# Performance work log

Hardware: AMD Instinct MI355X
Metric: run time of the kernel (lower is better)

## Reference

```python
import jax, jax.numpy as jnp
import numpy as np


def conv2d(x, w, b, pad):
    out = jax.lax.conv_general_dilated(x, w, (1, 1), ((pad, pad), (pad, pad)),
                                       dimension_numbers=('NCHW', 'OIHW', 'NCHW'))
    return out + b[None, :, None, None]


def silu(x):
    return x * jax.nn.sigmoid(x)


def group_norm(x, g, b, groups, eps=1e-5):
    B, C, H, W = x.shape
    xg = x.reshape(B, groups, C // groups, H, W)
    m = xg.mean(axis=(2, 3, 4), keepdims=True)
    v = xg.var(axis=(2, 3, 4), keepdims=True)
    xg = (xg - m) * jax.lax.rsqrt(v + eps)
    return xg.reshape(B, C, H, W) * g[None, :, None, None] + b[None, :, None, None]


def snake_cumsum(off):
    # off: [B,K,H,W]. Center kernel point has zero offset; points accumulate
    # outward from center (the 'snake' bend), as in DSCNet.
    K = off.shape[1]
    c = K // 2
    upper = jnp.cumsum(off[:, c + 1:], axis=1)
    lower = jnp.flip(jnp.cumsum(jnp.flip(off[:, :c], axis=1), axis=1), axis=1)
    return jnp.concatenate([lower, jnp.zeros_like(off[:, :1]), upper], axis=1)


def bilinear_gather(img, ys, xs):
    # img [B,C,H,W]; ys,xs [B,K,H,W] float coords -> sampled [B,C,K,H,W]
    B, C, H, W = img.shape
    K = ys.shape[1]
    ys = jnp.clip(ys, 0.0, H - 1.0)
    xs = jnp.clip(xs, 0.0, W - 1.0)
    y0f = jnp.floor(ys)
    x0f = jnp.floor(xs)
    wy = (ys - y0f)[:, None]  # [B,1,K,H,W]
    wx = (xs - x0f)[:, None]
    y0 = y0f.astype(jnp.int32)
    x0 = x0f.astype(jnp.int32)
    y1 = jnp.minimum(y0 + 1, H - 1)
    x1 = jnp.minimum(x0 + 1, W - 1)
    flat = img.reshape(B, C, H * W)

    def gat(yi, xi):
        idx = (yi * W + xi).reshape(B, -1)  # [B, K*H*W]
        g = jnp.take_along_axis(flat, idx[:, None, :], axis=2)
        return g.reshape(B, C, K, H, W)

    return (gat(y0, x0) * (1 - wy) * (1 - wx) + gat(y0, x1) * (1 - wy) * wx
            + gat(y1, x0) * wy * (1 - wx) + gat(y1, x1) * wy * wx)


def dsconv(x, off_w, off_b, dsc_w, dsc_b, gn_g, gn_b, morph, extend_scope=1.0):
    # Dynamic snake conv for one morphology.
    # morph 0: kernel spreads along x, bends in y; morph 1: opposite.
    B, C, H, W = x.shape
    K = dsc_w.shape[-1]
    c = K // 2
    off = jnp.tanh(conv2d(x, off_w, off_b, pad=1))  # [B,2K,H,W]; BN folded into conv bias
    bend = snake_cumsum(off[:, :K] if morph == 0 else off[:, K:])  # [B,K,H,W]
    spread = (jnp.arange(K) - c).astype(x.dtype)[None, :, None, None]
    hh = jnp.arange(H, dtype=x.dtype)[None, None, :, None]
    ww = jnp.arange(W, dtype=x.dtype)[None, None, None, :]
    if morph == 0:
        ys = hh + extend_scope * bend
        xs = jnp.broadcast_to(ww + spread, ys.shape)
    else:
        xs = ww + extend_scope * bend
        ys = jnp.broadcast_to(hh + spread, xs.shape)
    sampled = bilinear_gather(x, ys, xs)  # [B,C,K,H,W]
    # k-point conv over the stacked snake axis == (K,1)/(1,K) conv with stride K
    out = jnp.einsum('bckhw,ock->bohw', sampled, dsc_w) + dsc_b[None, :, None, None]
    O = dsc_w.shape[0]
    return jax.nn.relu(group_norm(out, gn_g, gn_b, groups=O // 4))


def dysnake_conv(x, p):
    # DySnakeConv: standard conv + snake-x + snake-y, concat, 1x1 fuse
    kpad = p['conv0_w'].shape[-1] // 2
    a = silu(conv2d(x, p['conv0_w'], p['conv0_b'], pad=kpad))
    bx = dsconv(x, p['offx_w'], p['offx_b'], p['dscx_w'], p['dscx_b'], p['gnx_g'], p['gnx_b'], morph=0)
    by = dsconv(x, p['offy_w'], p['offy_b'], p['dscy_w'], p['dscy_b'], p['gny_g'], p['gny_b'], morph=1)
    cat = jnp.concatenate([a, bx, by], axis=1)  # [B,3*ouc,H,W]
    return silu(jnp.einsum('bchw,oc->bohw', cat, p['fuse_w']) + p['fuse_b'][None, :, None, None])


_PNAMES = ['conv0_w', 'conv0_b', 'offx_w', 'offx_b', 'dscx_w', 'dscx_b', 'gnx_g', 'gnx_b',
           'offy_w', 'offy_b', 'dscy_w', 'dscy_b', 'gny_g', 'gny_b', 'fuse_w', 'fuse_b']


def setup_inputs() -> dict:
    key = jax.random.key(0)
    ks = iter(jax.random.split(key, 64))

    def rn(shape, s=0.05):
        return jax.random.normal(next(ks), shape, dtype=jnp.float32) * s

    B, H, W = 8, 80, 80
    c1, c2, c_ = 256, 256, 128
    kk = 3

    def block(inc, ouc, pre):
        return {
            pre + 'conv0_w': rn((ouc, inc, kk, kk)), pre + 'conv0_b': rn((ouc,)),
            pre + 'offx_w': rn((2 * kk, inc, 3, 3)), pre + 'offx_b': rn((2 * kk,)),
            pre + 'dscx_w': rn((ouc, inc, kk)), pre + 'dscx_b': rn((ouc,)),
            pre + 'gnx_g': jnp.ones((ouc,), jnp.float32), pre + 'gnx_b': jnp.zeros((ouc,), jnp.float32),
            pre + 'offy_w': rn((2 * kk, inc, 3, 3)), pre + 'offy_b': rn((2 * kk,)),
            pre + 'dscy_w': rn((ouc, inc, kk)), pre + 'dscy_b': rn((ouc,)),
            pre + 'gny_g': jnp.ones((ouc,), jnp.float32), pre + 'gny_b': jnp.zeros((ouc,), jnp.float32),
            pre + 'fuse_w': rn((ouc, 3 * ouc)), pre + 'fuse_b': rn((ouc,)),
        }

    inp = {'x': jax.random.normal(next(ks), (B, c1, H, W), dtype=jnp.float32)}
    inp.update(block(c1, c_, 'cv1_'))
    inp.update(block(c_, c2, 'cv2_'))
    return inp


def reference(x, cv1_conv0_w, cv1_conv0_b, cv1_offx_w, cv1_offx_b, cv1_dscx_w, cv1_dscx_b,
              cv1_gnx_g, cv1_gnx_b, cv1_offy_w, cv1_offy_b, cv1_dscy_w, cv1_dscy_b,
              cv1_gny_g, cv1_gny_b, cv1_fuse_w, cv1_fuse_b,
              cv2_conv0_w, cv2_conv0_b, cv2_offx_w, cv2_offx_b, cv2_dscx_w, cv2_dscx_b,
              cv2_gnx_g, cv2_gnx_b, cv2_offy_w, cv2_offy_b, cv2_dscy_w, cv2_dscy_b,
              cv2_gny_g, cv2_gny_b, cv2_fuse_w, cv2_fuse_b):
    p1 = dict(zip(_PNAMES, (cv1_conv0_w, cv1_conv0_b, cv1_offx_w, cv1_offx_b, cv1_dscx_w, cv1_dscx_b,
                            cv1_gnx_g, cv1_gnx_b, cv1_offy_w, cv1_offy_b, cv1_dscy_w, cv1_dscy_b,
                            cv1_gny_g, cv1_gny_b, cv1_fuse_w, cv1_fuse_b)))
    p2 = dict(zip(_PNAMES, (cv2_conv0_w, cv2_conv0_b, cv2_offx_w, cv2_offx_b, cv2_dscx_w, cv2_dscx_b,
                            cv2_gnx_g, cv2_gnx_b, cv2_offy_w, cv2_offy_b, cv2_dscy_w, cv2_dscy_b,
                            cv2_gny_g, cv2_gny_b, cv2_fuse_w, cv2_fuse_b)))
    h = dysnake_conv(x, p1)
    h = dysnake_conv(h, p2)
    return x + h  # shortcut and c1 == c2
```

## Files before the change

kernel.cpp:

```cpp
#include <hip/hip_runtime.h>
#include <cstddef>

#define B_   8
#define H_   80
#define W_   80
#define HW   6400
#define W2   82
#define HW2  6724

typedef __attribute__((ext_vector_type(8)))  short short8;
typedef __attribute__((ext_vector_type(16))) float f32x16;

__device__ __forceinline__ float bf2f(ushort u) {
    return __uint_as_float(((unsigned)u) << 16);
}
__device__ __forceinline__ ushort f2bf(float f) {
    unsigned u = __float_as_uint(f);
    u += 0x7FFF + ((u >> 16) & 1);
    return (ushort)(u >> 16);
}
__device__ __forceinline__ f32x16 mfma16(short8 a, short8 b, f32x16 c) {
    return __builtin_amdgcn_mfma_f32_32x32x16_bf16(a, b, c, 0, 0, 0);
}
__device__ __forceinline__ void async16(const void* g, void* l) {
    __builtin_amdgcn_global_load_lds(
        (const __attribute__((address_space(1))) unsigned int*)g,
        (__attribute__((address_space(3))) unsigned int*)l, 16, 0, 0);
}
__device__ __forceinline__ const ushort* frag_ptr(const ushort* sbuf, int row, int c8l) {
    return sbuf + row * 64 + ((c8l ^ (row & 7)) << 3);
}

__global__ __launch_bounds__(256) void halo_zero2_kernel(
    ushort* __restrict__ xp1, ushort* __restrict__ xp2) {
    int idx = blockIdx.x * 256 + threadIdx.x;
    const int n1 = B_ * 324 * 32;
    const int n2 = B_ * 324 * 16;
    ushort* xp; int C, slots, i;
    if (idx < n1) { xp = xp1; C = 256; slots = 32; i = idx; }
    else if (idx < n1 + n2) { xp = xp2; C = 128; slots = 16; i = idx - n1; }
    else return;
    int sl = i % slots;
    int t = i / slots;
    int p = t % 324;
    int b = t / 324;
    int h, w;
    if (p < 164) { h = (p < 82) ? 0 : 81; w = p % 82; }
    else { int q = p - 164; w = (q < 80) ? 0 : 81; h = 1 + (q % 80); }
    *(uint4*)(xp + ((size_t)(b * HW2 + h * W2 + w)) * C + sl * 8) =
        make_uint4(0, 0, 0, 0);
}

__global__ __launch_bounds__(256) void transpose_x_kernel(
    const float* __restrict__ x, ushort* __restrict__ xp, int C) {
    __shared__ float s[64][65];
    int hw0 = blockIdx.x * 64, c0 = blockIdx.y * 64, b = blockIdx.z;
    int t = threadIdx.x;
    int hl = t & 63, cq = t >> 6;
    #pragma unroll
    for (int i = 0; i < 16; i++) {
        int cl = cq * 16 + i;
        s[cl][hl] = x[((size_t)(b * C + c0 + cl)) * HW + hw0 + hl];
    }
    __syncthreads();
    int cl = t & 63, hq = t >> 6;
    #pragma unroll
    for (int i = 0; i < 16; i++) {
        int hl2 = hq * 16 + i;
        int hw = hw0 + hl2;
        int h = hw / W_, w = hw - h * W_;
        xp[((size_t)(b * HW2 + (h + 1) * W2 + w + 1)) * C + c0 + cl] = f2bf(s[cl][hl2]);
    }
}

__global__ __launch_bounds__(256) void final_add_kernel(
    const float* __restrict__ x, const ushort* __restrict__ h2,
    float* __restrict__ out, int C) {
    __shared__ float s[64][65];
    int hw0 = blockIdx.x * 64, c0 = blockIdx.y * 64, b = blockIdx.z;
    int t = threadIdx.x;
    int cl = t & 63, hq = t >> 6;
    #pragma unroll
    for (int i = 0; i < 16; i++) {
        int hl = hq * 16 + i;
        s[cl][hl] = bf2f(h2[((size_t)(b * HW + hw0 + hl)) * C + c0 + cl]);
    }
    __syncthreads();
    int hl = t & 63, cq = t >> 6;
    #pragma unroll
    for (int i = 0; i < 16; i++) {
        int cl2 = cq * 16 + i;
        size_t o = ((size_t)(b * C + c0 + cl2)) * HW + hw0 + hl;
        out[o] = x[o] + s[cl2][hl];
    }
}

struct WJobs {
    const float* src[8];
    ushort* dst[8];
    int cin[8], t[8];
    int start[9];
};

__global__ __launch_bounds__(256) void wprep_all_kernel(WJobs J) {
    int idx = blockIdx.x * 256 + threadIdx.x;
    if (idx >= J.start[8]) return;
    int j = 0;
    #pragma unroll
    for (int k = 1; k < 8; k++) if (idx >= J.start[k]) j = k;
    int i = idx - J.start[j];
    int CIN = J.cin[j], T = J.t[j];
    int oc = i / (CIN * T);
    int r = i - oc * CIN * T;
    int ci = r / T, t_ = r - ci * T;
    J.dst[j][((size_t)oc * T + t_) * CIN + ci] = f2bf(J.src[j][i]);
}

__global__ void wprep_off_kernel(const float* __restrict__ wx_,
                                 const float* __restrict__ bx_,
                                 const float* __restrict__ wy_,
                                 const float* __restrict__ by_,
                                 ushort* __restrict__ dst,
                                 float* __restrict__ bdst, int CIN) {
    int idx = blockIdx.x * 256 + threadIdx.x;
    if (idx < 4) {
        const int chs[4] = {0, 2, 3, 5};
        bdst[idx] = (idx < 2) ? bx_[chs[idx]] : by_[chs[idx]];
    }
    if (idx >= 32 * 9 * CIN) return;
    int oc = idx / (9 * CIN);
    int r = idx - oc * 9 * CIN;
    int tap = r / CIN, ci = r - tap * CIN;
    float v = 0.f;
    if (oc < 4) {
        const int chs[4] = {0, 2, 3, 5};
        const float* src = (oc < 2) ? wx_ : wy_;
        v = src[((size_t)chs[oc] * CIN + ci) * 9 + tap];
    }
    dst[idx] = f2bf(v);
}

__global__ __launch_bounds__(256, 2) void off_conv_mfma_kernel(
    const ushort* __restrict__ xp, const ushort* __restrict__ wB,
    const float* __restrict__ bias, float* __restrict__ off4, int CIN) {
    __shared__ ushort s_x[162 * 64];
    __shared__ ushort s_w[144 * 64];
    int tid = threadIdx.x;
    int ty0 = (blockIdx.x / 5) * 16, tx0 = (blockIdx.x % 5) * 16;
    int b = blockIdx.y;
    int lane = tid & 63, wid = tid >> 6;
    int l31 = lane & 31, kg = lane >> 5;
    int pym[2], pxm[2];
    #pragma unroll
    for (int mf = 0; mf < 2; mf++) {
        int p = wid * 64 + mf * 32 + l31;
        pym[mf] = p >> 4; pxm[mf] = p & 15;
    }
    f32x16 acc[2] = {};
    for (int c0 = 0; c0 < CIN; c0 += 32) {
        __syncthreads();
        for (int u = tid; u < 1296; u += 256) {
            int pid = u >> 2, ci8 = u & 3;
            int r = pid / 18, c = pid - r * 18;
            int py = ty0 + r, px = tx0 + c;
            uint4 v = *(const uint4*)(xp + ((size_t)(b * HW2 + py * W2 + px)) * CIN
                                      + c0 + ci8 * 8);
            int row = pid >> 1;
            int phys = (((pid & 1) << 2) + ci8) ^ (row & 7);
            *(uint4*)(s_x + row * 64 + phys * 8) = v;
        }
        for (int cc = wid; cc < 18; cc += 4) {
            int L = cc * 64 + lane;
            int row = L >> 3, phys = L & 7;
            int logical = phys ^ (row & 7);
            int tap = row >> 4, ocp = row & 15;
            int oc = ocp * 2 + (logical >> 2), ci8 = logical & 3;
            async16(wB + ((size_t)oc * 9 + tap) * CIN + c0 + ci8 * 8,
                    s_w + (size_t)L * 8);
        }
        __syncthreads();
        #pragma unroll
        for (int tap = 0; tap < 9; tap++) {
            int dy = tap / 3, dx = tap - dy * 3;
            int wrow = tap * 16 + (l31 >> 1);
            #pragma unroll
            for (int ks = 0; ks < 2; ks++) {
                int blk = ks * 2 + kg;
                int wphys = (((l31 & 1) << 2) + blk) ^ (wrow & 7);
                short8 bfr = *(const short8*)(s_w + wrow * 64 + wphys * 8);
                #pragma unroll
                for (int mf = 0; mf < 2; mf++) {
                    int pix = (pym[mf] + dy) * 18 + (pxm[mf] + dx);
                    int xrow = pix >> 1;
                    int xphys = (((pix & 1) << 2) + blk) ^ (xrow & 7);
                    short8 afr = *(const short8*)(s_x + xrow * 64 + xphys * 8);
                    acc[mf] = mfma16(afr, bfr, acc[mf]);
                }
            }
        }
    }
    int oc = l31;
    if (oc < 4) {
        float bb = bias[oc];
        #pragma unroll
        for (int mf = 0; mf < 2; mf++) {
            #pragma unroll
            for (int reg = 0; reg < 16; reg++) {
                int row = (reg & 3) + 8 * (reg >> 2) + 4 * kg;
                int p = wid * 64 + mf * 32 + row;
                int y = ty0 + (p >> 4), x = tx0 + (p & 15);
                off4[((size_t)b * 4 + oc) * HW + y * W_ + x] = tanhf(acc[mf][reg] + bb);
            }
        }
    }
}

__global__ __launch_bounds__(256, 4) void convdsc_kernel(
    const ushort* __restrict__ xp,
    const ushort* __restrict__ wC, const float* __restrict__ biasC,
    ushort* __restrict__ outC,
    const float* __restrict__ off4,
    const ushort* __restrict__ Bwx, const float* __restrict__ biasx,
    ushort* __restrict__ outx,
    const ushort* __restrict__ Bwy, const float* __restrict__ biasy,
    ushort* __restrict__ outy, float* __restrict__ stat, int CIN, int OC) {
    __shared__ ushort s_a[128 * 64];
    __shared__ ushort s_b[128 * 64];
    __shared__ int   s_i0[3][128];
    __shared__ int   s_i1[3][128];
    __shared__ float s_wl[3][128];
    int tid = threadIdx.x;
    int m0 = blockIdx.x * 128, n0 = blockIdx.y * 128;
    int b = m0 / HW, hw0 = m0 - b * HW;
    int lane = tid & 63, wid = tid >> 6;
    int l31 = lane & 31, kg = lane >> 5;
    int wm = wid >> 1, wn = wid & 1;

    if (blockIdx.z == 0) {
        const ushort* xpb = xp + (size_t)b * HW2 * CIN;
        const ushort* asrc[4];
        #pragma unroll
        for (int j = 0; j < 4; j++) {
            int s = (wid * 4 + j) * 64 + lane;
            int r = s >> 3, c8p = s & 7;
            int c8l = c8p ^ (r & 7);
            int hw = hw0 + r;
            int h = hw / W_, w = hw - h * W_;
            asrc[j] = xpb + ((size_t)((h + 1) * W2 + (w + 1))) * CIN + c8l * 8;
        }
        f32x16 acc[2][2] = {};
        int K = 9 * CIN, nk = K >> 6;
        int tap = 0, cioff = 0;
        for (int kc = 0; kc < nk; kc++) {
            int kg64 = kc << 6;
            int dy = tap / 3, dx = tap - dy * 3;
            int soff = ((dy - 1) * W2 + (dx - 1)) * CIN + cioff;
            __syncthreads();
            #pragma unroll
            for (int j = 0; j < 4; j++) {
                int s = (wid * 4 + j) * 64 + lane;
                int r = s >> 3, c8p = s & 7;
                int c8l = c8p ^ (r & 7);
                async16(wC + (size_t)(n0 + r) * K + kg64 + c8l * 8, s_b + s * 8);
                async16(asrc[j] + soff, s_a + s * 8);
            }
            __syncthreads();
            #pragma unroll
            for (int ks = 0; ks < 4; ks++) {
                int c8l = ks * 2 + kg;
                short8 af0 = *(const short8*)frag_ptr(s_a, wm * 64 + l31, c8l);
                short8 af1 = *(const short8*)frag_ptr(s_a, wm * 64 + 32 + l31, c8l);
                short8 bf0 = *(const short8*)frag_ptr(s_b, wn * 64 + l31, c8l);
                short8 bf1 = *(const short8*)frag_ptr(s_b, wn * 64 + 32 + l31, c8l);
                acc[0][0] = mfma16(af0, bf0, acc[0][0]);
                acc[0][1] = mfma16(af0, bf1, acc[0][1]);
                acc[1][0] = mfma16(af1, bf0, acc[1][0]);
                acc[1][1] = mfma16(af1, bf1, acc[1][1]);
            }
            cioff += 64;
            if (cioff == CIN) { cioff = 0; tap++; }
        }
        #pragma unroll
        for (int nf = 0; nf < 2; nf++) {
            int n = n0 + wn * 64 + nf * 32 + l31;
            float bb = biasC[n];
            #pragma unroll
            for (int mf = 0; mf < 2; mf++) {
                #pragma unroll
                for (int reg = 0; reg < 16; reg++) {
                    int row = (reg & 3) + 8 * (reg >> 2) + 4 * kg;
                    int m = m0 + wm * 64 + mf * 32 + row;
                    float v = acc[mf][nf][reg] + bb;
                    v = v / (1.f + expf(-v));
                    outC[(size_t)m * OC + n] = f2bf(v);
                }
            }
        }
        return;
    }

    int morph = blockIdx.z - 1;
    const ushort* Bw = morph ? Bwy : Bwx;
    const float* bias = morph ? biasy : biasx;
    ushort* out = morph ? outy : outx;
    float* statm = stat + (size_t)morph * B_ * 256 * 2;
    for (int u = tid; u < 384; u += 256) {
        int k3 = u >> 7, r = u & 127;
        int hw = hw0 + r;
        int h = hw / W_, w = hw - h * W_;
        float bend = 0.f;
        if (k3 != 1) {
            int mp = (morph ? 2 : 0) + (k3 >> 1);
            bend = off4[((size_t)b * 4 + mp) * HW + hw];
        }
        int i0, i1; float wl;
        if (morph == 0) {
            float ys = fminf(fmaxf((float)h + bend, 0.f), 79.f);
            float y0f = floorf(ys); wl = ys - y0f;
            int y0 = (int)y0f, y1 = min(y0 + 1, 79);
            int xk = min(max(w + k3 - 1, 0), 79);
            i0 = (y0 + 1) * W2 + xk + 1; i1 = (y1 + 1) * W2 + xk + 1;
        } else {
            float xs = fminf(fmaxf((float)w + bend, 0.f), 79.f);
            float x0f = floorf(xs); wl = xs - x0f;
            int x0 = (int)x0f, x1 = min(x0 + 1, 79);
            int yk = min(max(h + k3 - 1, 0), 79);
            i0 = (yk + 1) * W2 + x0 + 1; i1 = (yk + 1) * W2 + x1 + 1;
        }
        s_i0[k3][r] = i0; s_i1[k3][r] = i1; s_wl[k3][r] = wl;
    }
    const ushort* xb = xp + (size_t)b * HW2 * CIN;
    const ushort* asrcC[4];
    #pragma unroll
    for (int j = 0; j < 4; j++) {
        int s = (wid * 4 + j) * 64 + lane;
        int r = s >> 3, c8p = s & 7;
        int c8l = c8p ^ (r & 7);
        int hw = hw0 + r;
        int h = hw / W_, w = hw - h * W_;
        asrcC[j] = xb + ((size_t)((h + 1) * W2 + (w + 1))) * CIN + c8l * 8;
    }
    f32x16 acc[2][2] = {};
    int K = 3 * CIN, nk = K >> 6;
    for (int kc = 0; kc < nk; kc++) {
        int kg64 = kc << 6;
        int k3 = kg64 / CIN;
        int cioff = kg64 - k3 * CIN;
        __syncthreads();
        #pragma unroll
        for (int j = 0; j < 4; j++) {
            int s = (wid * 4 + j) * 64 + lane;
            int r = s >> 3, c8p = s & 7;
            int c8l = c8p ^ (r & 7);
            async16(Bw + (size_t)(n0 + r) * K + kg64 + c8l * 8, s_b + s * 8);
        }
        if (k3 == 1) {
            #pragma unroll
            for (int j = 0; j < 4; j++) {
                int s = (wid * 4 + j) * 64 + lane;
                async16(asrcC[j] + cioff, s_a + s * 8);
            }
        } else {
            #pragma unroll
            for (int i = 0; i < 4; i++) {
                int s = i * 256 + tid;
                int r = s >> 3, c8p = s & 7;
                int c8l = c8p ^ (r & 7);
                int ci = cioff + c8l * 8;
                float wl = s_wl[k3][r];
                uint4 u0 = *(const uint4*)(xb + (size_t)s_i0[k3][r] * CIN + ci);
                uint4 u1 = *(const uint4*)(xb + (size_t)s_i1[k3][r] * CIN + ci);
                const ushort* p0 = (const ushort*)&u0;
                const ushort* p1 = (const ushort*)&u1;
                uint ov[4];
                #pragma unroll
                for (int j = 0; j < 4; j++) {
                    float a0 = bf2f(p0[2 * j]),     b0 = bf2f(p1[2 * j]);
                    float a1 = bf2f(p0[2 * j + 1]), b1 = bf2f(p1[2 * j + 1]);
                    float r0 = a0 + (b0 - a0) * wl;
                    float r1 = a1 + (b1 - a1) * wl;
                    asm("v_cvt_pk_bf16_f32 %0, %1, %2"
                        : "=v"(ov[j]) : "v"(r0), "v"(r1));
                }
                *(uint4*)(s_a + s * 8) = *(uint4*)ov;
            }
        }
        __syncthreads();
        #pragma unroll
        for (int ks = 0; ks < 4; ks++) {
            int c8l = ks * 2 + kg;
            short8 af0 = *(const short8*)frag_ptr(s_a, wm * 64 + l31, c8l);
            short8 af1 = *(const short8*)frag_ptr(s_a, wm * 64 + 32 + l31, c8l);
            short8 bf0 = *(const short8*)frag_ptr(s_b, wn * 64 + l31, c8l);
            short8 bf1 = *(const short8*)frag_ptr(s_b, wn * 64 + 32 + l31, c8l);
            acc[0][0] = mfma16(af0, bf0, acc[0][0]);
            acc[0][1] = mfma16(af0, bf1, acc[0][1]);
            acc[1][0] = mfma16(af1, bf0, acc[1][0]);
            acc[1][1] = mfma16(af1, bf1, acc[1][1]);
        }
    }
    #pragma unroll
    for (int nf = 0; nf < 2; nf++) {
        int n = n0 + wn * 64 + nf * 32 + l31;
        float bb = bias[n];
        float ssum = 0.f, ssq = 0.f;
        #pragma unroll
        for (int mf = 0; mf < 2; mf++) {
            #pragma unroll
            for (int reg = 0; reg < 16; reg++) {
                int row = (reg & 3) + 8 * (reg >> 2) + 4 * kg;
                int m = m0 + wm * 64 + mf * 32 + row;
                float v = acc[mf][nf][reg] + bb;
                ssum += v; ssq += v * v;
                out[(size_t)m * OC + n] = f2bf(v);
            }
        }
        ssum += __shfl_xor(ssum, 32);
        ssq  += __shfl_xor(ssq, 32);
        if (kg == 0) {
            float* st = statm + ((size_t)b * OC + n) * 2;
            atomicAdd(st, ssum);
            atomicAdd(st + 1, ssq);
        }
    }
}

__global__ __launch_bounds__(256, 4) void gemm128_kernel(
    const ushort* __restrict__ a0, const ushort* __restrict__ a1,
    const ushort* __restrict__ a2, int part_k,
    const ushort* __restrict__ Bw, int K, int N,
    const float* __restrict__ bias, ushort* __restrict__ out, int epi_silu,
    int out_pad) {
    __shared__ ushort s_a[128 * 64];
    __shared__ ushort s_b[128 * 64];
    int tid = threadIdx.x;
    int m0 = blockIdx.x * 128, n0 = blockIdx.y * 128;
    int lane = tid & 63, wid = tid >> 6;
    int l31 = lane & 31, kg = lane >> 5;
    int wm = wid >> 1, wn = wid & 1;
    f32x16 acc[2][2] = {};
    int nk = K >> 6;
    for (int kc = 0; kc < nk; kc++) {
        int kg64 = kc << 6;
        int part = kg64 / part_k;
        int koff = kg64 - part * part_k;
        const ushort* ap = (part == 0) ? a0 : (part == 1 ? a1 : a2);
        __syncthreads();
        #pragma unroll
        for (int j = 0; j < 4; j++) {
            int s = (wid * 4 + j) * 64 + lane;
            int r = s >> 3, c8p = s & 7;
            int c8l = c8p ^ (r & 7);
            async16(ap + (size_t)(m0 + r) * part_k + koff + c8l * 8, s_a + s * 8);
            async16(Bw + (size_t)(n0 + r) * K + kg64 + c8l * 8, s_b + s * 8);
        }
        __syncthreads();
        #pragma unroll
        for (int ks = 0; ks < 4; ks++) {
            int c8l = ks * 2 + kg;
            short8 af0 = *(const short8*)frag_ptr(s_a, wm * 64 + l31, c8l);
            short8 af1 = *(const short8*)frag_ptr(s_a, wm * 64 + 32 + l31, c8l);
            short8 bf0 = *(const short8*)frag_ptr(s_b, wn * 64 + l31, c8l);
            short8 bf1 = *(const short8*)frag_ptr(s_b, wn * 64 + 32 + l31, c8l);
            acc[0][0] = mfma16(af0, bf0, acc[0][0]);
            acc[0][1] = mfma16(af0, bf1, acc[0][1]);
            acc[1][0] = mfma16(af1, bf0, acc[1][0]);
            acc[1][1] = mfma16(af1, bf1, acc[1][1]);
        }
    }
    #pragma unroll
    for (int nf = 0; nf < 2; nf++) {
        int n = n0 + wn * 64 + nf * 32 + l31;
        float bb = bias[n];
        #pragma unroll
        for (int mf = 0; mf < 2; mf++) {
            #pragma unroll
            for (int reg = 0; reg < 16; reg++) {
                int row = (reg & 3) + 8 * (reg >> 2) + 4 * kg;
                int m = m0 + wm * 64 + mf * 32 + row;
                float v = acc[mf][nf][reg] + bb;
                if (epi_silu) v = v / (1.f + expf(-v));
                size_t mm = (size_t)m;
                if (out_pad) {
                    int bb_ = m / HW, hw = m - bb_ * HW;
                    int h = hw / W_, w = hw - h * W_;
                    mm = (size_t)bb_ * HW2 + (h + 1) * W2 + w + 1;
                }
                out[mm * N + n] = f2bf(v);
            }
        }
    }
}

__global__ void gn_finalize_kernel(const float* __restrict__ stat,
                                   const float* __restrict__ gx,
                                   const float* __restrict__ bx,
                                   const float* __restrict__ gy,
                                   const float* __restrict__ by,
                                   float* __restrict__ scx, float* __restrict__ shx,
                                   float* __restrict__ scy, float* __restrict__ shy,
                                   int C) {
    int idx = blockIdx.x * 256 + threadIdx.x;
    if (idx >= B_ * C) return;
    int which = blockIdx.y;
    const float* gamma = which ? gy : gx;
    const float* beta  = which ? by : bx;
    float* sc = which ? scy : scx;
    float* sh = which ? shy : shx;
    int b = idx / C, c = idx - b * C;
    const float* st = stat + (size_t)which * B_ * 256 * 2
                    + ((size_t)b * C + (c & ~3)) * 2;
    float s  = st[0] + st[2] + st[4] + st[6];
    float sq = st[1] + st[3] + st[5] + st[7];
    float mean = s / (4.f * HW);
    float var = sq / (4.f * HW) - mean * mean;
    float rs = rsqrtf(var + 1e-5f);
    float scale = rs * gamma[c];
    sc[idx] = scale;
    sh[idx] = beta[c] - mean * scale;
}

__global__ __launch_bounds__(256) void gn_apply_kernel(
    ushort* __restrict__ bqx, ushort* __restrict__ bqy,
    const float* __restrict__ scx, const float* __restrict__ shx,
    const float* __restrict__ scy, const float* __restrict__ shy, int C) {
    ushort* bq = blockIdx.y ? bqy : bqx;
    const float* sc = blockIdx.y ? scy : scx;
    const float* sh = blockIdx.y ? shy : shx;
    size_t e = ((size_t)blockIdx.x * 256 + threadIdx.x) * 8;
    int c = (int)(e % C);
    int b = (int)(e / ((size_t)HW * C));
    const float* scb = sc + (size_t)b * C + c;
    const float* shb = sh + (size_t)b * C + c;
    uint4 v = *(const uint4*)(bq + e);
    const ushort* sv = (const ushort*)&v;
    ushort tv[8];
    #pragma unroll
    for (int j = 0; j < 8; j++)
        tv[j] = f2bf(fmaxf(bf2f(sv[j]) * scb[j] + shb[j], 0.f));
    *(uint4*)(bq + e) = *(uint4*)tv;
}

struct BlkBuf {
    ushort *xp, *abuf, *bqx, *bqy, *hout;
    float *off4, *stat, *scx, *shx, *scy, *shy, *boff;
    ushort *wc, *wdx, *wdy, *wf, *woff;
};

static void run_block(const BlkBuf& B, int CIN, int OC,
                      const float* const* P, int out_pad, hipStream_t stream) {
    dim3 blk(256);
    hipMemsetAsync(B.stat, 0, (size_t)2 * B_ * 256 * 2 * 4, stream);
    off_conv_mfma_kernel<<<dim3(25, B_), blk, 0, stream>>>(
        B.xp, B.woff, B.boff, B.off4, CIN);
    convdsc_kernel<<<dim3(400, OC / 128, 3), blk, 0, stream>>>(
        B.xp, B.wc, P[1], B.abuf,
        B.off4, B.wdx, P[5], B.bqx, B.wdy, P[11], B.bqy, B.stat, CIN, OC);
    int fgrid = (B_ * OC + 255) / 256;
    gn_finalize_kernel<<<dim3(fgrid, 2), blk, 0, stream>>>(
        B.stat, P[6], P[7], P[12], P[13], B.scx, B.shx, B.scy, B.shy, OC);
    gn_apply_kernel<<<dim3((B_ * HW * OC) / 2048, 2), blk, 0, stream>>>(
        B.bqx, B.bqy, B.scx, B.shx, B.scy, B.shy, OC);
    gemm128_kernel<<<dim3(400, OC / 128), blk, 0, stream>>>(
        B.abuf, B.bqx, B.bqy, OC, B.wf, 3 * OC, OC, P[15], B.hout, 1, out_pad);
}

extern "C" void kernel_launch(void* const* d_in, const int* in_sizes, int n_in,
                              void* d_out, int out_size, void* d_ws, size_t ws_size,
                              hipStream_t stream) {
    const float* x = (const float*)d_in[0];
    const float* P1[16];
    const float* P2[16];
    for (int i = 0; i < 16; i++) {
        P1[i] = (const float*)d_in[1 + i];
        P2[i] = (const float*)d_in[17 + i];
    }
    char* base = (char*)d_ws;
    size_t off = 0;
    auto alloc = [&](size_t bytes) -> char* {
        off = (off + 255) & ~(size_t)255;
        char* p = base + off;
        off += bytes;
        return p;
    };
    ushort* xp1  = (ushort*)alloc((size_t)B_ * HW2 * 256 * 2);
    ushort* xp2  = (ushort*)alloc((size_t)B_ * HW2 * 128 * 2);
    ushort* abuf = (ushort*)alloc((size_t)B_ * HW * 256 * 2);
    ushort* bqx  = (ushort*)alloc((size_t)B_ * HW * 256 * 2);
    ushort* bqy  = (ushort*)alloc((size_t)B_ * HW * 256 * 2);
    float*  off4 = (float*)alloc((size_t)B_ * 4 * HW * 4);
    float*  stat = (float*)alloc((size_t)2 * B_ * 256 * 2 * 4);
    float*  scx  = (float*)alloc(B_ * 256 * 4);
    float*  shx  = (float*)alloc(B_ * 256 * 4);
    float*  scy  = (float*)alloc(B_ * 256 * 4);
    float*  shy  = (float*)alloc(B_ * 256 * 4);
    ushort* wc1  = (ushort*)alloc((size_t)128 * 9 * 256 * 2);
    ushort* wc2  = (ushort*)alloc((size_t)256 * 9 * 128 * 2);
    ushort* wdx1 = (ushort*)alloc((size_t)128 * 3 * 256 * 2);
    ushort* wdy1 = (ushort*)alloc((size_t)128 * 3 * 256 * 2);
    ushort* wdx2 = (ushort*)alloc((size_t)256 * 3 * 128 * 2);
    ushort* wdy2 = (ushort*)alloc((size_t)256 * 3 * 128 * 2);
    ushort* wf1  = (ushort*)alloc((size_t)128 * 384 * 2);
    ushort* wf2  = (ushort*)alloc((size_t)256 * 768 * 2);
    ushort* wo1  = (ushort*)alloc((size_t)32 * 9 * 256 * 2);
    ushort* wo2  = (ushort*)alloc((size_t)32 * 9 * 128 * 2);
    float*  bo1  = (float*)alloc(32 * 4);
    float*  bo2  = (float*)alloc(32 * 4);
    ushort* h2 = xp1;

    dim3 blk(256);
    {
        int total = B_ * 324 * 32 + B_ * 324 * 16;
        halo_zero2_kernel<<<(total + 255) / 256, blk, 0, stream>>>(xp1, xp2);
    }

    {
        WJobs J;
        const float* srcs[8] = {P1[0], P1[4], P1[10], P1[14],
                                P2[0], P2[4], P2[10], P2[14]};
        ushort* dsts[8] = {wc1, wdx1, wdy1, wf1, wc2, wdx2, wdy2, wf2};
        int cins[8] = {256, 256, 256, 384, 128, 128, 128, 768};
        int ts[8]   = {9, 3, 3, 1, 9, 3, 3, 1};
        int ocs[8]  = {128, 128, 128, 128, 256, 256, 256, 256};
        int acc = 0;
        for (int j = 0; j < 8; j++) {
            J.src[j] = srcs[j]; J.dst[j] = dsts[j];
            J.cin[j] = cins[j]; J.t[j] = ts[j];
            J.start[j] = acc;
            acc += ocs[j] * cins[j] * ts[j];
        }
        J.start[8] = acc;
        wprep_all_kernel<<<(acc + 255) / 256, blk, 0, stream>>>(J);
    }
    wprep_off_kernel<<<(32 * 9 * 256 + 255) / 256, blk, 0, stream>>>(
        P1[2], P1[3], P1[8], P1[9], wo1, bo1, 256);
    wprep_off_kernel<<<(32 * 9 * 128 + 255) / 256, blk, 0, stream>>>(
        P2[2], P2[3], P2[8], P2[9], wo2, bo2, 128);

    transpose_x_kernel<<<dim3(100, 4, B_), blk, 0, stream>>>(x, xp1, 256);

    BlkBuf B1 = {xp1, abuf, bqx, bqy, xp2, off4, stat, scx, shx, scy, shy,
                 bo1, wc1, wdx1, wdy1, wf1, wo1};
    run_block(B1, 256, 128, P1, 1, stream);

    BlkBuf B2 = {xp2, abuf, bqx, bqy, h2, off4, stat, scx, shx, scy, shy,
                 bo2, wc2, wdx2, wdy2, wf2, wo2};
    run_block(B2, 128, 256, P2, 0, stream);

    final_add_kernel<<<dim3(100, 4, B_), blk, 0, stream>>>(x, h2, (float*)d_out, 256);
}
```

Measured before the change: 522.1 us.

## Fuse group-norm apply into fuse GEMM A-load and keep snake indices in registers

Removes the separate gn_apply pass by applying the GroupNorm scale/shift and ReLU while the fuse GEMM loads the bqx/bqy parts into LDS, replacing async copies with synchronous load-transform-store for those K chunks. In convdsc, the per-row bilinear indices and weights move from shared arrays into registers computed per thread, and the occupancy hint rises from 4 to 5 blocks. This saves a full read-modify-write of the two branch activations, at the cost of losing async overlap for two thirds of the GEMM K loop and added register pressure.

After: 669.8 us. 28.3% more time.

```diff
diff --git a/kernel.cpp b/kernel.cpp
--- a/kernel.cpp
+++ b/kernel.cpp
@@ -215,7 +215,7 @@
     }
 }
 
-__global__ __launch_bounds__(256, 4) void convdsc_kernel(
+__global__ __launch_bounds__(256, 5) void convdsc_kernel(
     const ushort* __restrict__ xp,
     const ushort* __restrict__ wC, const float* __restrict__ biasC,
     ushort* __restrict__ outC,
@@ -226,9 +226,6 @@
     ushort* __restrict__ outy, float* __restrict__ stat, int CIN, int OC) {
     __shared__ ushort s_a[128 * 64];
     __shared__ ushort s_b[128 * 64];
-    __shared__ int   s_i0[3][128];
-    __shared__ int   s_i1[3][128];
-    __shared__ float s_wl[3][128];
     int tid = threadIdx.x;
     int m0 = blockIdx.x * 128, n0 = blockIdx.y * 128;
     int b = m0 / HW, hw0 = m0 - b * HW;
@@ -304,30 +301,35 @@
     const float* bias = morph ? biasy : biasx;
     ushort* out = morph ? outy : outx;
     float* statm = stat + (size_t)morph * B_ * 256 * 2;
-    for (int u = tid; u < 384; u += 256) {
-        int k3 = u >> 7, r = u & 127;
+    int i0a[4], i1a[4], i0c[4], i1c[4];
+    float wla[4], wlc[4];
+    #pragma unroll
+    for (int i = 0; i < 4; i++) {
+        int r = i * 32 + (tid >> 3);
         int hw = hw0 + r;
         int h = hw / W_, w = hw - h * W_;
-        float bend = 0.f;
-        if (k3 != 1) {
-            int mp = (morph ? 2 : 0) + (k3 >> 1);
-            bend = off4[((size_t)b * 4 + mp) * HW + hw];
-        }
-        int i0, i1; float wl;
-        if (morph == 0) {
-            float ys = fminf(fmaxf((float)h + bend, 0.f), 79.f);
-            float y0f = floorf(ys); wl = ys - y0f;
-            int y0 = (int)y0f, y1 = min(y0 + 1, 79);
-            int xk = min(max(w + k3 - 1, 0), 79);
-            i0 = (y0 + 1) * W2 + xk + 1; i1 = (y1 + 1) * W2 + xk + 1;
-        } else {
-            float xs = fminf(fmaxf((float)w + bend, 0.f), 79.f);
-            float x0f = floorf(xs); wl = xs - x0f;
-            int x0 = (int)x0f, x1 = min(x0 + 1, 79);
-            int yk = min(max(h + k3 - 1, 0), 79);
-            i0 = (yk + 1) * W2 + x0 + 1; i1 = (yk + 1) * W2 + x1 + 1;
-        }
-        s_i0[k3][r] = i0; s_i1[k3][r] = i1; s_wl[k3][r] = wl;
+        #pragma unroll
+        for (int kk = 0; kk < 2; kk++) {
+            int k3v = kk * 2;
+            int mp = (morph ? 2 : 0) + (k3v >> 1);
+            float bend = off4[((size_t)b * 4 + mp) * HW + hw];
+            int i0, i1; float wl;
+            if (morph == 0) {
+                float ys = fminf(fmaxf((float)h + bend, 0.f), 79.f);
+                float y0f = floorf(ys); wl = ys - y0f;
+                int y0 = (int)y0f, y1 = min(y0 + 1, 79);
+                int xk = min(max(w + k3v - 1, 0), 79);
+                i0 = (y0 + 1) * W2 + xk + 1; i1 = (y1 + 1) * W2 + xk + 1;
+            } else {
+                float xs = fminf(fmaxf((float)w + bend, 0.f), 79.f);
+                float x0f = floorf(xs); wl = xs - x0f;
+                int x0 = (int)x0f, x1 = min(x0 + 1, 79);
+                int yk = min(max(h + k3v - 1, 0), 79);
+                i0 = (yk + 1) * W2 + x0 + 1; i1 = (yk + 1) * W2 + x1 + 1;
+            }
+            if (kk == 0) { i0a[i] = i0; i1a[i] = i1; wla[i] = wl; }
+            else         { i0c[i] = i0; i1c[i] = i1; wlc[i] = wl; }
+        }
     }
     const ushort* xb = xp + (size_t)b * HW2 * CIN;
     const ushort* asrcC[4];
@@ -361,15 +363,18 @@
                 async16(asrcC[j] + cioff, s_a + s * 8);
             }
         } else {
+            bool lo = (k3 == 0);
             #pragma unroll
             for (int i = 0; i < 4; i++) {
                 int s = i * 256 + tid;
                 int r = s >> 3, c8p = s & 7;
                 int c8l = c8p ^ (r & 7);
                 int ci = cioff + c8l * 8;
-                float wl = s_wl[k3][r];
-                uint4 u0 = *(const uint4*)(xb + (size_t)s_i0[k3][r] * CIN + ci);
-                uint4 u1 = *(const uint4*)(xb + (size_t)s_i1[k3][r] * CIN + ci);
+                int i0 = lo ? i0a[i] : i0c[i];
+                int i1 = lo ? i1a[i] : i1c[i];
+                float wl = lo ? wla[i] : wlc[i];
+                uint4 u0 = *(const uint4*)(xb + (size_t)i0 * CIN + ci);
+                uint4 u1 = *(const uint4*)(xb + (size_t)i1 * CIN + ci);
                 const ushort* p0 = (const ushort*)&u0;
                 const ushort* p1 = (const ushort*)&u1;
                 uint ov[4];
@@ -429,12 +434,15 @@
     const ushort* __restrict__ a0, const ushort* __restrict__ a1,
     const ushort* __restrict__ a2, int part_k,
     const ushort* __restrict__ Bw, int K, int N,
-    const float* __restrict__ bias, ushort* __restrict__ out, int epi_silu,
-    int out_pad) {
+    const float* __restrict__ bias,
+    const float* __restrict__ scx, const float* __restrict__ shx,
+    const float* __restrict__ scy, const float* __restrict__ shy,
+    ushort* __restrict__ out, int epi_silu, int out_pad) {
     __shared__ ushort s_a[128 * 64];
     __shared__ ushort s_b[128 * 64];
     int tid = threadIdx.x;
     int m0 = blockIdx.x * 128, n0 = blockIdx.y * 128;
+    int b = m0 / HW;
     int lane = tid & 63, wid = tid >> 6;
     int l31 = lane & 31, kg = lane >> 5;
     int wm = wid >> 1, wn = wid & 1;
@@ -444,15 +452,55 @@
         int kg64 = kc << 6;
         int part = kg64 / part_k;
         int koff = kg64 - part * part_k;
-        const ushort* ap = (part == 0) ? a0 : (part == 1 ? a1 : a2);
         __syncthreads();
         #pragma unroll
         for (int j = 0; j < 4; j++) {
             int s = (wid * 4 + j) * 64 + lane;
             int r = s >> 3, c8p = s & 7;
             int c8l = c8p ^ (r & 7);
-            async16(ap + (size_t)(m0 + r) * part_k + koff + c8l * 8, s_a + s * 8);
             async16(Bw + (size_t)(n0 + r) * K + kg64 + c8l * 8, s_b + s * 8);
+        }
+        if (part == 0) {
+            #pragma unroll
+            for (int j = 0; j < 4; j++) {
+                int s = (wid * 4 + j) * 64 + lane;
+                int r = s >> 3, c8p = s & 7;
+                int c8l = c8p ^ (r & 7);
+                async16(a0 + (size_t)(m0 + r) * part_k + koff + c8l * 8,
+                        s_a + s * 8);
+            }
+        } else {
+            const ushort* ap = (part == 1) ? a1 : a2;
+            const float* scp = ((part == 1) ? scx : scy) + (size_t)b * part_k;
+            const float* shp = ((part == 1) ? shx : shy) + (size_t)b * part_k;
+            #pragma unroll
+            for (int i = 0; i < 4; i++) {
+                int s = i * 256 + tid;
+                int r = s >> 3, c8p = s & 7;
+                int c8l = c8p ^ (r & 7);
+                int ch = koff + c8l * 8;
+                uint4 u = *(const uint4*)(ap + (size_t)(m0 + r) * part_k + ch);
+                float4 c0 = *(const float4*)(scp + ch);
+                float4 c1 = *(const float4*)(scp + ch + 4);
+                float4 h0 = *(const float4*)(shp + ch);
+                float4 h1 = *(const float4*)(shp + ch + 4);
+                const ushort* pv = (const ushort*)&u;
+                uint ov[4];
+                float r0, r1;
+                r0 = fmaxf(bf2f(pv[0]) * c0.x + h0.x, 0.f);
+                r1 = fmaxf(bf2f(pv[1]) * c0.y + h0.y, 0.f);
+                asm("v_cvt_pk_bf16_f32 %0, %1, %2" : "=v"(ov[0]) : "v"(r0), "v"(r1));
+                r0 = fmaxf(bf2f(pv[2]) * c0.z + h0.z, 0.f);
+                r1 = fmaxf(bf2f(pv[3]) * c0.w + h0.w, 0.f);
+                asm("v_cvt_pk_bf16_f32 %0, %1, %2" : "=v"(ov[1]) : "v"(r0), "v"(r1));
+                r0 = fmaxf(bf2f(pv[4]) * c1.x + h1.x, 0.f);
+                r1 = fmaxf(bf2f(pv[5]) * c1.y + h1.y, 0.f);
+                asm("v_cvt_pk_bf16_f32 %0, %1, %2" : "=v"(ov[2]) : "v"(r0), "v"(r1));
+                r0 = fmaxf(bf2f(pv[6]) * c1.z + h1.z, 0.f);
+                r1 = fmaxf(bf2f(pv[7]) * c1.w + h1.w, 0.f);
+                asm("v_cvt_pk_bf16_f32 %0, %1, %2" : "=v"(ov[3]) : "v"(r0), "v"(r1));
+                *(uint4*)(s_a + s * 8) = *(uint4*)ov;
+            }
         }
         __syncthreads();
         #pragma unroll
@@ -520,27 +568,6 @@
     sh[idx] = beta[c] - mean * scale;
 }
 
-__global__ __launch_bounds__(256) void gn_apply_kernel(
-    ushort* __restrict__ bqx, ushort* __restrict__ bqy,
-    const float* __restrict__ scx, const float* __restrict__ shx,
-    const float* __restrict__ scy, const float* __restrict__ shy, int C) {
-    ushort* bq = blockIdx.y ? bqy : bqx;
-    const float* sc = blockIdx.y ? scy : scx;
-    const float* sh = blockIdx.y ? shy : shx;
-    size_t e = ((size_t)blockIdx.x * 256 + threadIdx.x) * 8;
-    int c = (int)(e % C);
-    int b = (int)(e / ((size_t)HW * C));
-    const float* scb = sc + (size_t)b * C + c;
-    const float* shb = sh + (size_t)b * C + c;
-    uint4 v = *(const uint4*)(bq + e);
-    const ushort* sv = (const ushort*)&v;
-    ushort tv[8];
-    #pragma unroll
-    for (int j = 0; j < 8; j++)
-        tv[j] = f2bf(fmaxf(bf2f(sv[j]) * scb[j] + shb[j], 0.f));
-    *(uint4*)(bq + e) = *(uint4*)tv;
-}
-
 struct BlkBuf {
     ushort *xp, *abuf, *bqx, *bqy, *hout;
     float *off4, *stat, *scx, *shx, *scy, *shy, *boff;
@@ -559,10 +586,9 @@
     int fgrid = (B_ * OC + 255) / 256;
     gn_finalize_kernel<<<dim3(fgrid, 2), blk, 0, stream>>>(
         B.stat, P[6], P[7], P[12], P[13], B.scx, B.shx, B.scy, B.shy, OC);
-    gn_apply_kernel<<<dim3((B_ * HW * OC) / 2048, 2), blk, 0, stream>>>(
-        B.bqx, B.bqy, B.scx, B.shx, B.scy, B.shy, OC);
     gemm128_kernel<<<dim3(400, OC / 128), blk, 0, stream>>>(
-        B.abuf, B.bqx, B.bqy, OC, B.wf, 3 * OC, OC, P[15], B.hout, 1, out_pad);
+        B.abuf, B.bqx, B.bqy, OC, B.wf, 3 * OC, OC, P[15],
+        B.scx, B.shx, B.scy, B.shy, B.hout, 1, out_pad);
 }
 
 extern "C" void kernel_launch(void* const* d_in, const int* in_sizes, int n_in,
```
